# Optimization experiments

Measured on AMD Instinct MI355X. Metric: run time of the kernel, lower is better.

## Reference

```python
import jax, jax.numpy as jnp
import numpy as np

EPS = 1e-10


def setup_inputs() -> dict:
    key = jax.random.key(0)
    k1, k2 = jax.random.split(key)
    supports = jax.random.normal(k1, (32, 512, 1024), dtype=jnp.float32)
    targets = jax.random.normal(k2, (32, 512, 1024), dtype=jnp.float32)
    return {"supports": supports, "targets": targets}


def reference(supports, targets):
    # targets: [B, T, D], supports: [B, S, D] -> sim: [B, T, S]
    # F.cosine_similarity(a, b, eps): dot / max(||a||*||b||, eps)
    dots = jnp.einsum("btd,bsd->bts", targets, supports)
    t_norm = jnp.linalg.norm(targets, axis=-1)   # [B, T]
    s_norm = jnp.linalg.norm(supports, axis=-1)  # [B, S]
    denom = jnp.maximum(t_norm[:, :, None] * s_norm[:, None, :], EPS)
    sim = dots / denom
    # normalize=True default: map (-1, 1) -> (0, 1)
    return (sim + 1.0) * 0.5
```

## Files before the change

### kernel.cpp

```cpp
#include <hip/hip_runtime.h>
#include <hip/hip_bf16.h>

typedef __attribute__((ext_vector_type(8))) short short8;
typedef __attribute__((ext_vector_type(4))) short short4b;
typedef __attribute__((ext_vector_type(4))) float f32x4;

#define NBATCH 32
#define NT 512
#define NS 512
#define ND 1024
#define BM 128
#define BN 128
#define BK 32
#define NK (ND / BK)

__device__ __forceinline__ short f2bf(float f) {
    union { __hip_bfloat16 h; short s; } u;
    u.h = __float2bfloat16(f);
    return u.s;
}

__device__ __forceinline__ short4b cvt4(float4 a) {
    short4b r;
    r[0] = f2bf(a.x); r[1] = f2bf(a.y); r[2] = f2bf(a.z); r[3] = f2bf(a.w);
    return r;
}

__device__ __forceinline__ float ssq4(float s, float4 a) {
    return fmaf(a.x, a.x, fmaf(a.y, a.y, fmaf(a.z, a.z, fmaf(a.w, a.w, s))));
}

__global__ __launch_bounds__(512, 4)
void paircos_mfma(const float* __restrict__ sup, const float* __restrict__ tgt,
                  float* __restrict__ out) {
    __shared__ __align__(16) short As[2][BM * BK];
    __shared__ __align__(16) short Bs[2][BN * BK];
    __shared__ float tn[BM];
    __shared__ float sn[BN];

    const int tid = threadIdx.x;
    const int l    = blockIdx.x;
    const int wgid = (l & 7) * 64 + (l >> 3);
    const int b    = wgid >> 4;
    const int til  = wgid & 15;
    const int bt0  = (til >> 2) * BM;
    const int bs0  = (til & 3) * BN;

    const int c8 = tid & 7;
    const int r0 = tid >> 3;

    const float* gA = tgt + (size_t)b * NT * ND + (size_t)(bt0 + r0) * ND + c8 * 4;
    const float* gB = sup + (size_t)b * NS * ND + (size_t)(bs0 + r0) * ND + c8 * 4;

    const int wave = tid >> 6;
    const int lane = tid & 63;
    const int wr  = (wave >> 2) * 64;
    const int wc  = (wave & 3) * 32;
    const int lhi = lane >> 4;
    const int llo = lane & 15;

    f32x4 acc[4][2];
#pragma unroll
    for (int m = 0; m < 4; ++m)
#pragma unroll
        for (int n = 0; n < 2; ++n)
            acc[m][n] = (f32x4){0.f, 0.f, 0.f, 0.f};

    float sqa0 = 0.f, sqa1 = 0.f, sqb0 = 0.f, sqb1 = 0.f;

    float4 eA0, eA1, eB0, eB1, oA0, oA1, oB0, oB1;

    const int u0   = ((c8 >> 1) + (r0 >> 1)) & 3;
    const int off0 = r0 * BK + u0 * 8 + (c8 & 1) * 4;
    const int off1 = (r0 + 64) * BK + u0 * 8 + (c8 & 1) * 4;

#define LOADT(A0, A1, B0, B1, KK)                                              \
    do {                                                                       \
        A0 = *reinterpret_cast<const float4*>(gA + (KK) * BK);                 \
        A1 = *reinterpret_cast<const float4*>(gA + (KK) * BK + 64 * ND);       \
        B0 = *reinterpret_cast<const float4*>(gB + (KK) * BK);                 \
        B1 = *reinterpret_cast<const float4*>(gB + (KK) * BK + 64 * ND);       \
    } while (0)

#define STORET(A0, A1, B0, B1, P)                                              \
    do {                                                                       \
        sqa0 = ssq4(sqa0, A0); *reinterpret_cast<short4b*>(&As[P][off0]) = cvt4(A0); \
        sqa1 = ssq4(sqa1, A1); *reinterpret_cast<short4b*>(&As[P][off1]) = cvt4(A1); \
        sqb0 = ssq4(sqb0, B0); *reinterpret_cast<short4b*>(&Bs[P][off0]) = cvt4(B0); \
        sqb1 = ssq4(sqb1, B1); *reinterpret_cast<short4b*>(&Bs[P][off1]) = cvt4(B1); \
    } while (0)

#define COMPUTE(P)                                                             \
    do {                                                                       \
        short8 af[4], bfr[2];                                                  \
        _Pragma("unroll") for (int m = 0; m < 4; ++m) {                        \
            const int row = wr + m * 16 + llo;                                 \
            const int off = row * BK + (((lhi + (row >> 1)) & 3) * 8);         \
            af[m] = *reinterpret_cast<const short8*>(&As[P][off]);             \
        }                                                                      \
        _Pragma("unroll") for (int n = 0; n < 2; ++n) {                        \
            const int row = wc + n * 16 + llo;                                 \
            const int off = row * BK + (((lhi + (row >> 1)) & 3) * 8);         \
            bfr[n] = *reinterpret_cast<const short8*>(&Bs[P][off]);            \
        }                                                                      \
        _Pragma("unroll") for (int m = 0; m < 4; ++m)                          \
            _Pragma("unroll") for (int n = 0; n < 2; ++n)                      \
                acc[m][n] = __builtin_amdgcn_mfma_f32_16x16x32_bf16(           \
                    af[m], bfr[n], acc[m][n], 0, 0, 0);                        \
    } while (0)

#define PHASE_FENCE()                                                          \
    do {                                                                       \
        asm volatile("s_waitcnt lgkmcnt(0)" ::: "memory");                     \
        __builtin_amdgcn_s_barrier();                                          \
        asm volatile("" ::: "memory");                                         \
    } while (0)

    LOADT(eA0, eA1, eB0, eB1, 0);
    STORET(eA0, eA1, eB0, eB1, 0);
    LOADT(eA0, eA1, eB0, eB1, 1);
    LOADT(oA0, oA1, oB0, oB1, 2);
    PHASE_FENCE();

    for (int k = 0; k < NK; k += 2) {
        STORET(eA0, eA1, eB0, eB1, 1);
        if (k + 3 < NK) LOADT(eA0, eA1, eB0, eB1, k + 3);
        COMPUTE(0);
        PHASE_FENCE();
        if (k + 2 < NK) STORET(oA0, oA1, oB0, oB1, 0);
        if (k + 4 < NK) LOADT(oA0, oA1, oB0, oB1, k + 4);
        COMPUTE(1);
        PHASE_FENCE();
    }

#pragma unroll
    for (int d = 1; d < 8; d <<= 1) {
        sqa0 += __shfl_xor(sqa0, d);
        sqa1 += __shfl_xor(sqa1, d);
        sqb0 += __shfl_xor(sqb0, d);
        sqb1 += __shfl_xor(sqb1, d);
    }
    if (c8 == 0) {
        tn[r0]      = sqrtf(sqa0);
        tn[r0 + 64] = sqrtf(sqa1);
        sn[r0]      = sqrtf(sqb0);
        sn[r0 + 64] = sqrtf(sqb1);
    }
    __syncthreads();

    float* outp = out + (size_t)b * NT * NS;
#pragma unroll
    for (int m = 0; m < 4; ++m) {
        const int lr0 = wr + m * 16 + lhi * 4;
#pragma unroll
        for (int n = 0; n < 2; ++n) {
            const int lc = wc + n * 16 + llo;
            const float snv = sn[lc];
            const int col = bs0 + lc;
#pragma unroll
            for (int j = 0; j < 4; ++j) {
                const float denom = fmaxf(tn[lr0 + j] * snv, 1e-10f);
                outp[(size_t)(bt0 + lr0 + j) * NS + col] =
                    acc[m][n][j] / denom * 0.5f + 0.5f;
            }
        }
    }
}

extern "C" void kernel_launch(void* const* d_in, const int* in_sizes, int n_in,
                              void* d_out, int out_size, void* d_ws, size_t ws_size,
                              hipStream_t stream) {
    const float* sup = (const float*)d_in[0];
    const float* tgt = (const float*)d_in[1];
    float* out = (float*)d_out;
    (void)in_sizes; (void)n_in; (void)out_size; (void)d_ws; (void)ws_size;
    paircos_mfma<<<dim3(16 * NBATCH), 512, 0, stream>>>(sup, tgt, out);
}
```

Before: 39.67 us.

## Use 256-thread blocks with 64x64 per-wave tiles

Halves the workgroup to 4 waves, so each wave now computes a 64x64 output sub-tile (4x4 MFMA tiles) rather than 64x32, and each thread loads 4 rows of A and B per K-step. This raises MFMA work per LDS fragment load and cuts barrier participants per block. In exchange, per-thread register use grows (more accumulators and prefetch buffers), fewer waves hide global-load latency, and the launch bound drops to 2 blocks per CU.

```diff
diff --git a/kernel.cpp b/kernel.cpp
--- a/kernel.cpp
+++ b/kernel.cpp
@@ -30,7 +30,7 @@
     return fmaf(a.x, a.x, fmaf(a.y, a.y, fmaf(a.z, a.z, fmaf(a.w, a.w, s))));
 }
 
-__global__ __launch_bounds__(512, 4)
+__global__ __launch_bounds__(256, 2)
 void paircos_mfma(const float* __restrict__ sup, const float* __restrict__ tgt,
                   float* __restrict__ out) {
     __shared__ __align__(16) short As[2][BM * BK];
@@ -54,57 +54,59 @@
 
     const int wave = tid >> 6;
     const int lane = tid & 63;
-    const int wr  = (wave >> 2) * 64;
-    const int wc  = (wave & 3) * 32;
+    const int wr  = (wave >> 1) * 64;
+    const int wc  = (wave & 1) * 64;
     const int lhi = lane >> 4;
     const int llo = lane & 15;
 
-    f32x4 acc[4][2];
+    f32x4 acc[4][4];
 #pragma unroll
     for (int m = 0; m < 4; ++m)
 #pragma unroll
-        for (int n = 0; n < 2; ++n)
+        for (int n = 0; n < 4; ++n)
             acc[m][n] = (f32x4){0.f, 0.f, 0.f, 0.f};
 
-    float sqa0 = 0.f, sqa1 = 0.f, sqb0 = 0.f, sqb1 = 0.f;
+    float sqa[4] = {0.f, 0.f, 0.f, 0.f};
+    float sqb[4] = {0.f, 0.f, 0.f, 0.f};
 
-    float4 eA0, eA1, eB0, eB1, oA0, oA1, oB0, oB1;
+    float4 eA[4], eB[4], oA[4], oB[4];
 
     const int u0   = ((c8 >> 1) + (r0 >> 1)) & 3;
     const int off0 = r0 * BK + u0 * 8 + (c8 & 1) * 4;
-    const int off1 = (r0 + 64) * BK + u0 * 8 + (c8 & 1) * 4;
 
-#define LOADT(A0, A1, B0, B1, KK)                                              \
+#define LOADT(RA, RB, KK)                                                      \
     do {                                                                       \
-        A0 = *reinterpret_cast<const float4*>(gA + (KK) * BK);                 \
-        A1 = *reinterpret_cast<const float4*>(gA + (KK) * BK + 64 * ND);       \
-        B0 = *reinterpret_cast<const float4*>(gB + (KK) * BK);                 \
-        B1 = *reinterpret_cast<const float4*>(gB + (KK) * BK + 64 * ND);       \
+        _Pragma("unroll") for (int j = 0; j < 4; ++j) {                        \
+            RA[j] = *reinterpret_cast<const float4*>(gA + (KK) * BK + (size_t)j * 32 * ND); \
+            RB[j] = *reinterpret_cast<const float4*>(gB + (KK) * BK + (size_t)j * 32 * ND); \
+        }                                                                      \
     } while (0)
 
-#define STORET(A0, A1, B0, B1, P)                                              \
+#define STORET(RA, RB, P)                                                      \
     do {                                                                       \
-        sqa0 = ssq4(sqa0, A0); *reinterpret_cast<short4b*>(&As[P][off0]) = cvt4(A0); \
-        sqa1 = ssq4(sqa1, A1); *reinterpret_cast<short4b*>(&As[P][off1]) = cvt4(A1); \
-        sqb0 = ssq4(sqb0, B0); *reinterpret_cast<short4b*>(&Bs[P][off0]) = cvt4(B0); \
-        sqb1 = ssq4(sqb1, B1); *reinterpret_cast<short4b*>(&Bs[P][off1]) = cvt4(B1); \
+        _Pragma("unroll") for (int j = 0; j < 4; ++j) {                        \
+            sqa[j] = ssq4(sqa[j], RA[j]);                                      \
+            *reinterpret_cast<short4b*>(&As[P][off0 + j * 32 * BK]) = cvt4(RA[j]); \
+            sqb[j] = ssq4(sqb[j], RB[j]);                                      \
+            *reinterpret_cast<short4b*>(&Bs[P][off0 + j * 32 * BK]) = cvt4(RB[j]); \
+        }                                                                      \
     } while (0)
 
 #define COMPUTE(P)                                                             \
     do {                                                                       \
-        short8 af[4], bfr[2];                                                  \
+        short8 af[4], bfr[4];                                                  \
         _Pragma("unroll") for (int m = 0; m < 4; ++m) {                        \
             const int row = wr + m * 16 + llo;                                 \
             const int off = row * BK + (((lhi + (row >> 1)) & 3) * 8);         \
             af[m] = *reinterpret_cast<const short8*>(&As[P][off]);             \
         }                                                                      \
-        _Pragma("unroll") for (int n = 0; n < 2; ++n) {                        \
+        _Pragma("unroll") for (int n = 0; n < 4; ++n) {                        \
             const int row = wc + n * 16 + llo;                                 \
             const int off = row * BK + (((lhi + (row >> 1)) & 3) * 8);         \
             bfr[n] = *reinterpret_cast<const short8*>(&Bs[P][off]);            \
         }                                                                      \
         _Pragma("unroll") for (int m = 0; m < 4; ++m)                          \
-            _Pragma("unroll") for (int n = 0; n < 2; ++n)                      \
+            _Pragma("unroll") for (int n = 0; n < 4; ++n)                      \
                 acc[m][n] = __builtin_amdgcn_mfma_f32_16x16x32_bf16(           \
                     af[m], bfr[n], acc[m][n], 0, 0, 0);                        \
     } while (0)
@@ -116,35 +118,37 @@
         asm volatile("" ::: "memory");                                         \
     } while (0)
 
-    LOADT(eA0, eA1, eB0, eB1, 0);
-    STORET(eA0, eA1, eB0, eB1, 0);
-    LOADT(eA0, eA1, eB0, eB1, 1);
-    LOADT(oA0, oA1, oB0, oB1, 2);
+    LOADT(eA, eB, 0);
+    STORET(eA, eB, 0);
+    LOADT(eA, eB, 1);
+    LOADT(oA, oB, 2);
     PHASE_FENCE();
 
     for (int k = 0; k < NK; k += 2) {
-        STORET(eA0, eA1, eB0, eB1, 1);
-        if (k + 3 < NK) LOADT(eA0, eA1, eB0, eB1, k + 3);
+        STORET(eA, eB, 1);
+        if (k + 3 < NK) LOADT(eA, eB, k + 3);
         COMPUTE(0);
         PHASE_FENCE();
-        if (k + 2 < NK) STORET(oA0, oA1, oB0, oB1, 0);
-        if (k + 4 < NK) LOADT(oA0, oA1, oB0, oB1, k + 4);
+        if (k + 2 < NK) STORET(oA, oB, 0);
+        if (k + 4 < NK) LOADT(oA, oB, k + 4);
         COMPUTE(1);
         PHASE_FENCE();
     }
 
 #pragma unroll
     for (int d = 1; d < 8; d <<= 1) {
-        sqa0 += __shfl_xor(sqa0, d);
-        sqa1 += __shfl_xor(sqa1, d);
-        sqb0 += __shfl_xor(sqb0, d);
-        sqb1 += __shfl_xor(sqb1, d);
+#pragma unroll
+        for (int j = 0; j < 4; ++j) {
+            sqa[j] += __shfl_xor(sqa[j], d);
+            sqb[j] += __shfl_xor(sqb[j], d);
+        }
     }
     if (c8 == 0) {
-        tn[r0]      = sqrtf(sqa0);
-        tn[r0 + 64] = sqrtf(sqa1);
-        sn[r0]      = sqrtf(sqb0);
-        sn[r0 + 64] = sqrtf(sqb1);
+#pragma unroll
+        for (int j = 0; j < 4; ++j) {
+            tn[r0 + j * 32] = sqrtf(sqa[j]);
+            sn[r0 + j * 32] = sqrtf(sqb[j]);
+        }
     }
     __syncthreads();
 
@@ -153,7 +157,7 @@
     for (int m = 0; m < 4; ++m) {
         const int lr0 = wr + m * 16 + lhi * 4;
 #pragma unroll
-        for (int n = 0; n < 2; ++n) {
+        for (int n = 0; n < 4; ++n) {
             const int lc = wc + n * 16 + llo;
             const float snv = sn[lc];
             const int col = bs0 + lc;
@@ -174,5 +178,5 @@
     const float* tgt = (const float*)d_in[1];
     float* out = (float*)d_out;
     (void)in_sizes; (void)n_in; (void)out_size; (void)d_ws; (void)ws_size;
-    paircos_mfma<<<dim3(16 * NBATCH), 512, 0, stream>>>(sup, tgt, out);
+    paircos_mfma<<<dim3(16 * NBATCH), 256, 0, stream>>>(sup, tgt, out);
 }
```

Measured after the change: 41.86 us. +5.5%, slower.

## Widen LDS stores to 16 bytes, read fragments early, raise MFMA priority

Applied to the files above, without the earlier changes.

Each thread now loads 8 contiguous floats from one row instead of 4 floats from two rows, then writes one 16-byte bf16 vector to LDS using the same swizzle the fragment reads use. Fragment reads from LDS are issued before the store and global-load phase, so LDS latency overlaps with the conversions, and the MFMA block is wrapped in s_setprio. The norm reduction shrinks to a 4-lane shuffle. This costs more live registers and the global access pattern changes to 32-byte segments per thread.

```diff
diff --git a/kernel.cpp b/kernel.cpp
--- a/kernel.cpp
+++ b/kernel.cpp
@@ -2,7 +2,6 @@
 #include <hip/hip_bf16.h>
 
 typedef __attribute__((ext_vector_type(8))) short short8;
-typedef __attribute__((ext_vector_type(4))) short short4b;
 typedef __attribute__((ext_vector_type(4))) float f32x4;
 
 #define NBATCH 32
@@ -20,9 +19,10 @@
     return u.s;
 }
 
-__device__ __forceinline__ short4b cvt4(float4 a) {
-    short4b r;
+__device__ __forceinline__ short8 cvt8(float4 a, float4 b) {
+    short8 r;
     r[0] = f2bf(a.x); r[1] = f2bf(a.y); r[2] = f2bf(a.z); r[3] = f2bf(a.w);
+    r[4] = f2bf(b.x); r[5] = f2bf(b.y); r[6] = f2bf(b.z); r[7] = f2bf(b.w);
     return r;
 }
 
@@ -46,11 +46,11 @@
     const int bt0  = (til >> 2) * BM;
     const int bs0  = (til & 3) * BN;
 
-    const int c8 = tid & 7;
-    const int r0 = tid >> 3;
+    const int seg  = tid & 3;
+    const int srow = tid >> 2;
 
-    const float* gA = tgt + (size_t)b * NT * ND + (size_t)(bt0 + r0) * ND + c8 * 4;
-    const float* gB = sup + (size_t)b * NS * ND + (size_t)(bs0 + r0) * ND + c8 * 4;
+    const float* gA = tgt + (size_t)b * NT * ND + (size_t)(bt0 + srow) * ND + seg * 8;
+    const float* gB = sup + (size_t)b * NS * ND + (size_t)(bs0 + srow) * ND + seg * 8;
 
     const int wave = tid >> 6;
     const int lane = tid & 63;
@@ -66,33 +66,30 @@
         for (int n = 0; n < 2; ++n)
             acc[m][n] = (f32x4){0.f, 0.f, 0.f, 0.f};
 
-    float sqa0 = 0.f, sqa1 = 0.f, sqb0 = 0.f, sqb1 = 0.f;
+    float sqa = 0.f, sqb = 0.f;
 
     float4 eA0, eA1, eB0, eB1, oA0, oA1, oB0, oB1;
 
-    const int u0   = ((c8 >> 1) + (r0 >> 1)) & 3;
-    const int off0 = r0 * BK + u0 * 8 + (c8 & 1) * 4;
-    const int off1 = (r0 + 64) * BK + u0 * 8 + (c8 & 1) * 4;
+    const int offw = srow * BK + (((seg + (srow >> 1)) & 3) * 8);
 
 #define LOADT(A0, A1, B0, B1, KK)                                              \
     do {                                                                       \
         A0 = *reinterpret_cast<const float4*>(gA + (KK) * BK);                 \
-        A1 = *reinterpret_cast<const float4*>(gA + (KK) * BK + 64 * ND);       \
+        A1 = *reinterpret_cast<const float4*>(gA + (KK) * BK + 4);             \
         B0 = *reinterpret_cast<const float4*>(gB + (KK) * BK);                 \
-        B1 = *reinterpret_cast<const float4*>(gB + (KK) * BK + 64 * ND);       \
+        B1 = *reinterpret_cast<const float4*>(gB + (KK) * BK + 4);             \
     } while (0)
 
 #define STORET(A0, A1, B0, B1, P)                                              \
     do {                                                                       \
-        sqa0 = ssq4(sqa0, A0); *reinterpret_cast<short4b*>(&As[P][off0]) = cvt4(A0); \
-        sqa1 = ssq4(sqa1, A1); *reinterpret_cast<short4b*>(&As[P][off1]) = cvt4(A1); \
-        sqb0 = ssq4(sqb0, B0); *reinterpret_cast<short4b*>(&Bs[P][off0]) = cvt4(B0); \
-        sqb1 = ssq4(sqb1, B1); *reinterpret_cast<short4b*>(&Bs[P][off1]) = cvt4(B1); \
+        sqa = ssq4(ssq4(sqa, A0), A1);                                         \
+        *reinterpret_cast<short8*>(&As[P][offw]) = cvt8(A0, A1);               \
+        sqb = ssq4(ssq4(sqb, B0), B1);                                         \
+        *reinterpret_cast<short8*>(&Bs[P][offw]) = cvt8(B0, B1);               \
     } while (0)
 
-#define COMPUTE(P)                                                             \
+#define FRAG_READ(P)                                                           \
     do {                                                                       \
-        short8 af[4], bfr[2];                                                  \
         _Pragma("unroll") for (int m = 0; m < 4; ++m) {                        \
             const int row = wr + m * 16 + llo;                                 \
             const int off = row * BK + (((lhi + (row >> 1)) & 3) * 8);         \
@@ -103,10 +100,16 @@
             const int off = row * BK + (((lhi + (row >> 1)) & 3) * 8);         \
             bfr[n] = *reinterpret_cast<const short8*>(&Bs[P][off]);            \
         }                                                                      \
+    } while (0)
+
+#define MFMA_BLOCK()                                                           \
+    do {                                                                       \
+        __builtin_amdgcn_s_setprio(1);                                         \
         _Pragma("unroll") for (int m = 0; m < 4; ++m)                          \
             _Pragma("unroll") for (int n = 0; n < 2; ++n)                      \
                 acc[m][n] = __builtin_amdgcn_mfma_f32_16x16x32_bf16(           \
                     af[m], bfr[n], acc[m][n], 0, 0, 0);                        \
+        __builtin_amdgcn_s_setprio(0);                                         \
     } while (0)
 
 #define PHASE_FENCE()                                                          \
@@ -123,28 +126,31 @@
     PHASE_FENCE();
 
     for (int k = 0; k < NK; k += 2) {
-        STORET(eA0, eA1, eB0, eB1, 1);
-        if (k + 3 < NK) LOADT(eA0, eA1, eB0, eB1, k + 3);
-        COMPUTE(0);
-        PHASE_FENCE();
-        if (k + 2 < NK) STORET(oA0, oA1, oB0, oB1, 0);
-        if (k + 4 < NK) LOADT(oA0, oA1, oB0, oB1, k + 4);
-        COMPUTE(1);
-        PHASE_FENCE();
+        {
+            short8 af[4], bfr[2];
+            FRAG_READ(0);
+            STORET(eA0, eA1, eB0, eB1, 1);
+            if (k + 3 < NK) LOADT(eA0, eA1, eB0, eB1, k + 3);
+            MFMA_BLOCK();
+            PHASE_FENCE();
+        }
+        {
+            short8 af[4], bfr[2];
+            FRAG_READ(1);
+            if (k + 2 < NK) STORET(oA0, oA1, oB0, oB1, 0);
+            if (k + 4 < NK) LOADT(oA0, oA1, oB0, oB1, k + 4);
+            MFMA_BLOCK();
+            PHASE_FENCE();
+        }
     }
 
-#pragma unroll
-    for (int d = 1; d < 8; d <<= 1) {
-        sqa0 += __shfl_xor(sqa0, d);
-        sqa1 += __shfl_xor(sqa1, d);
-        sqb0 += __shfl_xor(sqb0, d);
-        sqb1 += __shfl_xor(sqb1, d);
-    }
-    if (c8 == 0) {
-        tn[r0]      = sqrtf(sqa0);
-        tn[r0 + 64] = sqrtf(sqa1);
-        sn[r0]      = sqrtf(sqb0);
-        sn[r0 + 64] = sqrtf(sqb1);
+    sqa += __shfl_xor(sqa, 1);
+    sqa += __shfl_xor(sqa, 2);
+    sqb += __shfl_xor(sqb, 1);
+    sqb += __shfl_xor(sqb, 2);
+    if (seg == 0) {
+        tn[srow] = sqrtf(sqa);
+        sn[srow] = sqrtf(sqb);
     }
     __syncthreads();
 
```

Measured after the change: 39.30 us. Within noise of the previous version (-0.9%).
